# Performance work log

Hardware: AMD Instinct MI355X
Metric: run time of the kernel (lower is better)

Reference implementation:

```python
import jax, jax.numpy as jnp
import numpy as np

EMBED = 1024
B, S = 4, 4096

def setup_inputs() -> dict:
    key = jax.random.key(0)
    ks = jax.random.split(key, 7)
    std = 1.0 / np.sqrt(EMBED)
    X = jax.random.normal(ks[0], (B, S, EMBED), dtype=jnp.float32)
    Wq = jax.random.uniform(ks[1], (EMBED, EMBED), jnp.float32, -std, std)
    bq = jax.random.uniform(ks[2], (EMBED,), jnp.float32, -std, std)
    Wk = jax.random.uniform(ks[3], (EMBED, EMBED), jnp.float32, -std, std)
    bk = jax.random.uniform(ks[4], (EMBED,), jnp.float32, -std, std)
    Wv = jax.random.uniform(ks[5], (EMBED, EMBED), jnp.float32, -std, std)
    bv = jax.random.uniform(ks[6], (EMBED,), jnp.float32, -std, std)
    return {"X": X, "Wq": Wq, "bq": bq, "Wk": Wk, "bk": bk, "Wv": Wv, "bv": bv}

def reference(X, Wq, bq, Wk, bk, Wv, bv):
    # Linear layers (torch convention: x @ W.T + b)
    q = X @ Wq.T + bq  # [B, S, E]
    k = X @ Wk.T + bk
    v = X @ Wv.T + bv
    scale = 1.0 / jnp.sqrt(jnp.asarray(EMBED, X.dtype))
    scores = jnp.einsum('bse,bte->bst', q, k) * scale  # [B, S, S]
    weights = jax.nn.softmax(scores, axis=-1)
    return jnp.einsum('bst,bte->bse', weights, v)  # [B, S, E]
```

## Files before the change

kernel.cpp:

```cpp
#include <hip/hip_runtime.h>
#include <stdint.h>


typedef unsigned short ushort_t;
typedef __attribute__((ext_vector_type(8))) short short8;
typedef __attribute__((ext_vector_type(4))) float f32x4;

__device__ inline ushort_t f2bf(float f) {
  union { float f; unsigned u; } v; v.f = f;
  unsigned r = v.u + 0x7fffu + ((v.u >> 16) & 1u);
  return (ushort_t)(r >> 16);
}

__global__ __launch_bounds__(256) void zero_f32(float* __restrict__ p, int n) {
  int i = blockIdx.x * 256 + threadIdx.x;
  if (i < n) p[i] = 0.0f;
}

__global__ __launch_bounds__(256) void cvt_f32_bf16(
    const float* __restrict__ in, ushort_t* __restrict__ out, int n4) {
  int i = blockIdx.x * 256 + threadIdx.x;
  if (i < n4) {
    float4 v = ((const float4*)in)[i];
    ushort4 o;
    o.x = f2bf(v.x); o.y = f2bf(v.y); o.z = f2bf(v.z); o.w = f2bf(v.w);
    ((ushort4*)out)[i] = o;
  }
}

#define BM 256
#define BN 256
#define BK 64

template<int EPI>
__global__ __launch_bounds__(512, 2) void gemm_nt(
    const ushort_t* __restrict__ A, const ushort_t* __restrict__ B,
    const float* __restrict__ aux, const float* __restrict__ aux2,
    void* __restrict__ Cv,
    int K, int ldc, float scale, long sA, long sB, long sC,
    int lstride, float* __restrict__ lsum) {
  __shared__ ushort_t As[2][2][128 * 64];
  __shared__ ushort_t Bs[2][2][128 * 64];

  const int t = threadIdx.x;
  const int lane = t & 63;
  const int wave = t >> 6;
  const int wr = wave >> 2;
  const int wc = wave & 3;
  const int lr = lane & 15;
  const int quad = lane >> 4;

  const int gx = gridDim.x;
  const int nwg = gx * gridDim.y;
  const int lin = blockIdx.y * gx + blockIdx.x;
  const int swz = (lin & 7) * (nwg >> 3) + (lin >> 3);
  const int m0 = (swz / gx) * BM;
  const int n0 = (swz % gx) * BN;

  const long z = blockIdx.z;
  A += z * sA;
  B += z * sB;

  const int srow = t >> 3;
  const int scol = ((t & 7) ^ (srow & 7)) << 3;
  const ushort_t* pA = A + (size_t)(m0 + srow) * K + scol;
  const ushort_t* pB = B + (size_t)(n0 + srow) * K + scol;

  const int nkt = K / BK;

#define GLL(gp, lp) __builtin_amdgcn_global_load_lds( \
    (const __attribute__((address_space(1))) void*)(gp), \
    (__attribute__((address_space(3))) void*)(lp), 16, 0, 0)

#define STAGE_A(b, h, kt) do { if ((kt) < nkt) { \
    const ushort_t* g_ = pA + (size_t)(h) * 128 * K + (size_t)(kt) * BK; \
    GLL(g_, &As[b][h][t * 8]); \
    GLL(g_ + (size_t)64 * K, &As[b][h][(512 + t) * 8]); } } while (0)

#define STAGE_B(b, h, kt) do { if ((kt) < nkt) { \
    const ushort_t* g_ = pB + (size_t)(h) * 128 * K + (size_t)(kt) * BK; \
    GLL(g_, &Bs[b][h][t * 8]); \
    GLL(g_ + (size_t)64 * K, &Bs[b][h][(512 + t) * 8]); } } while (0)

  int aoff[4], boff[2];
#pragma unroll
  for (int mi = 0; mi < 4; ++mi)
    aoff[mi] = (wr * 64 + mi * 16 + lr) * 64 + ((quad ^ (lr & 7)) << 3);
#pragma unroll
  for (int ni = 0; ni < 2; ++ni)
    boff[ni] = (wc * 32 + ni * 16 + lr) * 64 + ((quad ^ (lr & 7)) << 3);

  f32x4 acc[8][4] = {};
  short8 af[4][2], bf[2][2];

#define LDA(b, mh) do { \
  _Pragma("unroll") for (int mi_ = 0; mi_ < 4; ++mi_) { \
    af[mi_][0] = *(const short8*)&As[b][mh][aoff[mi_]]; \
    af[mi_][1] = *(const short8*)&As[b][mh][aoff[mi_] ^ 32]; } } while (0)

#define LDB(b, nh) do { \
  _Pragma("unroll") for (int ni_ = 0; ni_ < 2; ++ni_) { \
    bf[ni_][0] = *(const short8*)&Bs[b][nh][boff[ni_]]; \
    bf[ni_][1] = *(const short8*)&Bs[b][nh][boff[ni_] ^ 32]; } } while (0)

#define MFMA16(mh, nh) do { \
  _Pragma("unroll") for (int mi_ = 0; mi_ < 4; ++mi_) \
  _Pragma("unroll") for (int ni_ = 0; ni_ < 2; ++ni_) { \
    acc[(mh) * 4 + mi_][(nh) * 2 + ni_] = __builtin_amdgcn_mfma_f32_16x16x32_bf16( \
        af[mi_][0], bf[ni_][0], acc[(mh) * 4 + mi_][(nh) * 2 + ni_], 0, 0, 0); \
    acc[(mh) * 4 + mi_][(nh) * 2 + ni_] = __builtin_amdgcn_mfma_f32_16x16x32_bf16( \
        af[mi_][1], bf[ni_][1], acc[(mh) * 4 + mi_][(nh) * 2 + ni_], 0, 0, 0); } } while (0)

#define PH_TAIL \
  __builtin_amdgcn_s_barrier(); \
  asm volatile("s_waitcnt lgkmcnt(0)" ::: "memory"); \
  __builtin_amdgcn_sched_barrier(0); \
  __builtin_amdgcn_s_setprio(1)

#define PH_END \
  __builtin_amdgcn_s_setprio(0); \
  __builtin_amdgcn_s_barrier()

  STAGE_A(0, 0, 0); STAGE_B(0, 0, 0); STAGE_A(0, 1, 0); STAGE_B(0, 1, 0);
  asm volatile("s_waitcnt vmcnt(4)" ::: "memory");
  STAGE_A(1, 0, 1); STAGE_B(1, 0, 1); STAGE_A(1, 1, 1);
  asm volatile("s_waitcnt vmcnt(6)" ::: "memory");
  __builtin_amdgcn_s_barrier();

  const int iters = nkt >> 1;
  for (int it = 0; it < iters; ++it) {
    const int T = it * 2;
    const bool last = (it == iters - 1);

    LDA(0, 0); LDB(0, 0);
    STAGE_B(1, 1, T + 1);
    PH_TAIL; MFMA16(0, 0); PH_END;

    LDB(0, 1);
    STAGE_A(0, 0, T + 2);
    PH_TAIL; MFMA16(0, 1); PH_END;

    LDA(0, 1); LDB(0, 0);
    STAGE_B(0, 0, T + 2);
    PH_TAIL; MFMA16(1, 0); PH_END;

    LDB(0, 1);
    STAGE_A(0, 1, T + 2);
    PH_TAIL; MFMA16(1, 1);
    __builtin_amdgcn_s_setprio(0);
    if (last) asm volatile("s_waitcnt vmcnt(0)" ::: "memory");
    else      asm volatile("s_waitcnt vmcnt(6)" ::: "memory");
    __builtin_amdgcn_s_barrier();

    LDA(1, 0); LDB(1, 0);
    STAGE_B(0, 1, T + 2);
    PH_TAIL; MFMA16(0, 0); PH_END;

    LDB(1, 1);
    STAGE_A(1, 0, T + 3);
    PH_TAIL; MFMA16(0, 1); PH_END;

    LDA(1, 1); LDB(1, 0);
    STAGE_B(1, 0, T + 3);
    PH_TAIL; MFMA16(1, 0); PH_END;

    LDB(1, 1);
    STAGE_A(1, 1, T + 3);
    PH_TAIL; MFMA16(1, 1);
    __builtin_amdgcn_s_setprio(0);
    if (!last) asm volatile("s_waitcnt vmcnt(6)" ::: "memory");
    __builtin_amdgcn_s_barrier();
  }

  const float* bias = (EPI == 1 && z) ? aux2 : aux;
#pragma unroll
  for (int fm = 0; fm < 8; ++fm) {
#pragma unroll
    for (int r = 0; r < 4; ++r) {
      const int row = m0 + (fm >> 2) * 128 + wr * 64 + (fm & 3) * 16 + quad * 4 + r;
      float rs = 0.0f, rl = 0.0f;
      if (EPI == 4) rl = 1.0f / bias[(size_t)z * lstride + row];
#pragma unroll
      for (int fn = 0; fn < 4; ++fn) {
        const int col = n0 + (fn >> 1) * 128 + wc * 32 + (fn & 1) * 16 + lr;
        const size_t off = (size_t)(z * sC) + (size_t)row * ldc + col;
        float v = acc[fm][fn][r] * scale;
        if (EPI == 1) {
          ((ushort_t*)Cv)[off] = f2bf(v + bias[col]);
        } else if (EPI == 2) {
          ((ushort_t*)Cv)[off] = f2bf(v + bias[row]);
        } else if (EPI == 3) {
          float e = __expf(v);
          rs += e;
          ((ushort_t*)Cv)[off] = f2bf(e);
        } else {
          ((float*)Cv)[off] = v * rl;
        }
      }
      if (EPI == 3) {
        rs += __shfl_xor(rs, 1);
        rs += __shfl_xor(rs, 2);
        rs += __shfl_xor(rs, 4);
        rs += __shfl_xor(rs, 8);
        if (lr == 0)
          atomicAdd(&lsum[(size_t)z * lstride + row], rs);
      }
    }
  }
}

extern "C" void kernel_launch(void* const* d_in, const int* in_sizes, int n_in,
                              void* d_out, int out_size, void* d_ws,
                              size_t ws_size, hipStream_t stream) {
  const float* X  = (const float*)d_in[0];
  const float* Wq = (const float*)d_in[1];
  const float* bq = (const float*)d_in[2];
  const float* Wk = (const float*)d_in[3];
  const float* bk = (const float*)d_in[4];
  const float* Wv = (const float*)d_in[5];
  const float* bv = (const float*)d_in[6];
  float* out = (float*)d_out;

  const int Bn = 4, S = 4096, E = 1024;
  const long SE  = (long)S * E;
  const long BSE = (long)Bn * SE;
  const long SS  = (long)S * S;
  const long EE  = (long)E * E;

  const size_t need_batched =
      (size_t)(4 * SS + 3 * EE + 3 * BSE) * 2 + (size_t)Bn * S * 4;
  const bool batched = ws_size >= need_batched;

  const long front = batched ? 4 * SS : BSE;
  ushort_t* Xb  = (ushort_t*)d_ws;
  ushort_t* P   = (ushort_t*)d_ws;
  ushort_t* Wqb = (ushort_t*)d_ws + front;
  ushort_t* Wkb = Wqb + EE;
  ushort_t* Wvb = Wkb + EE;
  ushort_t* Qw  = Wvb + EE;
  ushort_t* Kw  = Qw + BSE;
  ushort_t* Vt  = Kw + BSE;
  float*    l   = (float*)(Vt + BSE);

  zero_f32<<<(Bn * S) / 256, 256, 0, stream>>>(l, Bn * S);

  cvt_f32_bf16<<<(int)(BSE / 1024), 256, 0, stream>>>(X, Xb, (int)(BSE / 4));
  cvt_f32_bf16<<<(int)(EE / 1024), 256, 0, stream>>>(Wq, Wqb, (int)(EE / 4));
  cvt_f32_bf16<<<(int)(EE / 1024), 256, 0, stream>>>(Wk, Wkb, (int)(EE / 4));
  cvt_f32_bf16<<<(int)(EE / 1024), 256, 0, stream>>>(Wv, Wvb, (int)(EE / 4));

  gemm_nt<1><<<dim3(E / BN, Bn * S / BM, 2), 512, 0, stream>>>(
      Xb, Wqb, bq, bk, Qw, E, E, 1.0f, 0, EE, BSE, 0, nullptr);

  gemm_nt<2><<<dim3(S / BN, E / BM, Bn), 512, 0, stream>>>(
      Wvb, Xb, bv, nullptr, Vt, E, S, 1.0f, 0, SE, SE, 0, nullptr);

  if (batched) {
    gemm_nt<3><<<dim3(S / BN, S / BM, Bn), 512, 0, stream>>>(
        Qw, Kw, nullptr, nullptr, P, E, S, 0.03125f, SE, SE, SS, S, l);
    gemm_nt<4><<<dim3(E / BN, S / BM, Bn), 512, 0, stream>>>(
        P, Vt, l, nullptr, out, S, E, 1.0f, SS, SE, SE, S, nullptr);
  } else {
    for (int b = 0; b < Bn; ++b) {
      gemm_nt<3><<<dim3(S / BN, S / BM), 512, 0, stream>>>(
          Qw + b * SE, Kw + b * SE, nullptr, nullptr, P, E, S, 0.03125f,
          0, 0, 0, 0, l + b * S);
      gemm_nt<4><<<dim3(E / BN, S / BM), 512, 0, stream>>>(
          P, Vt + b * SE, l + b * S, nullptr, out + b * SE, S, E, 1.0f,
          0, 0, 0, 0, nullptr);
    }
  }
}
```

Measured before the change: 537.3 us.

## Make GEMM kernel persistent with cross-tile prefetch and XCD-chunked scheduling

Converts the GEMM into a persistent kernel launched with 256 workgroups, each processing several output tiles in sequence. Global-to-LDS staging for the next tile begins during the tail of the current tile's K-loop, which hides the prologue load latency between tiles. Tiles are assigned in chunks per XCD for cache locality. It also switches to 32-bit byte offsets, reorders the staging so B halves are held in separate register buffers, and trims redundant LDS reads. The risks are higher register pressure, 32-bit offset overflow on large tensors, and load imbalance.

```diff
diff --git a/kernel.cpp b/kernel.cpp
--- a/kernel.cpp
+++ b/kernel.cpp
@@ -3,6 +3,7 @@
 
 
 typedef unsigned short ushort_t;
+typedef unsigned int uint_t;
 typedef __attribute__((ext_vector_type(8))) short short8;
 typedef __attribute__((ext_vector_type(4))) float f32x4;
 
@@ -38,7 +39,8 @@
     const float* __restrict__ aux, const float* __restrict__ aux2,
     void* __restrict__ Cv,
     int K, int ldc, float scale, long sA, long sB, long sC,
-    int lstride, float* __restrict__ lsum) {
+    int lstride, float* __restrict__ lsum,
+    int tn, int tm, int tz, int tpb) {
   __shared__ ushort_t As[2][2][128 * 64];
   __shared__ ushort_t Bs[2][2][128 * 64];
 
@@ -50,37 +52,64 @@
   const int lr = lane & 15;
   const int quad = lane >> 4;
 
-  const int gx = gridDim.x;
-  const int nwg = gx * gridDim.y;
-  const int lin = blockIdx.y * gx + blockIdx.x;
-  const int swz = (lin & 7) * (nwg >> 3) + (lin >> 3);
-  const int m0 = (swz / gx) * BM;
-  const int n0 = (swz % gx) * BN;
-
-  const long z = blockIdx.z;
-  A += z * sA;
-  B += z * sB;
+  const int Kb = K * 2;
+  const int nkt = K / BK;
+  const int niter = nkt >> 1;
 
   const int srow = t >> 3;
   const int scol = ((t & 7) ^ (srow & 7)) << 3;
-  const ushort_t* pA = A + (size_t)(m0 + srow) * K + scol;
-  const ushort_t* pB = B + (size_t)(n0 + srow) * K + scol;
-
-  const int nkt = K / BK;
+
+  const int NT = tn * tm * tz;
+  const int tmn = tn * tm;
+  const bool chunked = (gridDim.x == 256) && ((NT & 255) == 0);
+  const int xcd = blockIdx.x & 7, wblk = blockIdx.x >> 3;
+  const int cpx = NT >> 3;
+
+  auto calc = [&](int i, int& m0_, int& n0_, long& z_, uint_t& oa_, uint_t& ob_) {
+    const int lin = chunked ? (xcd * cpx + i * 32 + wblk)
+                            : ((int)blockIdx.x + i * (int)gridDim.x);
+    const int zz = lin / tmn;
+    const int r = lin - zz * tmn;
+    const int mi = r / tn;
+    const int ni = r - mi * tn;
+    m0_ = mi * BM; n0_ = ni * BN; z_ = zz;
+    oa_ = (uint_t)(((size_t)zz * (size_t)sA + (size_t)(m0_ + srow) * K + scol) * 2);
+    ob_ = (uint_t)(((size_t)zz * (size_t)sB + (size_t)(n0_ + srow) * K + scol) * 2);
+  };
+
+  int m0, n0, m0n, n0n;
+  long z, zn;
+  uint_t oA_cur, oB_cur, oA_nxt, oB_nxt;
+  calc(0, m0, n0, z, oA_cur, oB_cur);
+  bool have_next = (tpb > 1);
+  if (have_next) calc(1, m0n, n0n, zn, oA_nxt, oB_nxt);
+  else { m0n = m0; n0n = n0; zn = z; oA_nxt = oA_cur; oB_nxt = oB_cur; }
 
 #define GLL(gp, lp) __builtin_amdgcn_global_load_lds( \
     (const __attribute__((address_space(1))) void*)(gp), \
     (__attribute__((address_space(3))) void*)(lp), 16, 0, 0)
 
-#define STAGE_A(b, h, kt) do { if ((kt) < nkt) { \
-    const ushort_t* g_ = pA + (size_t)(h) * 128 * K + (size_t)(kt) * BK; \
-    GLL(g_, &As[b][h][t * 8]); \
-    GLL(g_ + (size_t)64 * K, &As[b][h][(512 + t) * 8]); } } while (0)
-
-#define STAGE_B(b, h, kt) do { if ((kt) < nkt) { \
-    const ushort_t* g_ = pB + (size_t)(h) * 128 * K + (size_t)(kt) * BK; \
-    GLL(g_, &Bs[b][h][t * 8]); \
-    GLL(g_ + (size_t)64 * K, &Bs[b][h][(512 + t) * 8]); } } while (0)
+#define STAGE_A(b, h, j) do { \
+    const int j_ = (j); \
+    const bool in_ = (j_ < nkt); \
+    if (in_ || have_next) { \
+      const uint_t o_ = (in_ ? (oA_cur + (uint_t)(j_ * 128)) \
+                             : (oA_nxt + (uint_t)((j_ - nkt) * 128))) \
+                        + (uint_t)((h) * 128 * Kb); \
+      const char* g_ = (const char*)A + o_; \
+      GLL(g_, &As[b][h][t * 8]); \
+      GLL(g_ + (size_t)64 * Kb, &As[b][h][(512 + t) * 8]); } } while (0)
+
+#define STAGE_B(b, h, j) do { \
+    const int j_ = (j); \
+    const bool in_ = (j_ < nkt); \
+    if (in_ || have_next) { \
+      const uint_t o_ = (in_ ? (oB_cur + (uint_t)(j_ * 128)) \
+                             : (oB_nxt + (uint_t)((j_ - nkt) * 128))) \
+                        + (uint_t)((h) * 128 * Kb); \
+      const char* g_ = (const char*)B + o_; \
+      GLL(g_, &Bs[b][h][t * 8]); \
+      GLL(g_ + (size_t)64 * Kb, &Bs[b][h][(512 + t) * 8]); } } while (0)
 
   int aoff[4], boff[2];
 #pragma unroll
@@ -91,7 +120,8 @@
     boff[ni] = (wc * 32 + ni * 16 + lr) * 64 + ((quad ^ (lr & 7)) << 3);
 
   f32x4 acc[8][4] = {};
-  short8 af[4][2], bf[2][2];
+  short8 af[4][2];
+  short8 bfr[2][2][2];
 
 #define LDA(b, mh) do { \
   _Pragma("unroll") for (int mi_ = 0; mi_ < 4; ++mi_) { \
@@ -100,16 +130,16 @@
 
 #define LDB(b, nh) do { \
   _Pragma("unroll") for (int ni_ = 0; ni_ < 2; ++ni_) { \
-    bf[ni_][0] = *(const short8*)&Bs[b][nh][boff[ni_]]; \
-    bf[ni_][1] = *(const short8*)&Bs[b][nh][boff[ni_] ^ 32]; } } while (0)
+    bfr[nh][ni_][0] = *(const short8*)&Bs[b][nh][boff[ni_]]; \
+    bfr[nh][ni_][1] = *(const short8*)&Bs[b][nh][boff[ni_] ^ 32]; } } while (0)
 
 #define MFMA16(mh, nh) do { \
   _Pragma("unroll") for (int mi_ = 0; mi_ < 4; ++mi_) \
   _Pragma("unroll") for (int ni_ = 0; ni_ < 2; ++ni_) { \
     acc[(mh) * 4 + mi_][(nh) * 2 + ni_] = __builtin_amdgcn_mfma_f32_16x16x32_bf16( \
-        af[mi_][0], bf[ni_][0], acc[(mh) * 4 + mi_][(nh) * 2 + ni_], 0, 0, 0); \
+        af[mi_][0], bfr[nh][ni_][0], acc[(mh) * 4 + mi_][(nh) * 2 + ni_], 0, 0, 0); \
     acc[(mh) * 4 + mi_][(nh) * 2 + ni_] = __builtin_amdgcn_mfma_f32_16x16x32_bf16( \
-        af[mi_][1], bf[ni_][1], acc[(mh) * 4 + mi_][(nh) * 2 + ni_], 0, 0, 0); } } while (0)
+        af[mi_][1], bfr[nh][ni_][1], acc[(mh) * 4 + mi_][(nh) * 2 + ni_], 0, 0, 0); } } while (0)
 
 #define PH_TAIL \
   __builtin_amdgcn_s_barrier(); \
@@ -121,90 +151,100 @@
   __builtin_amdgcn_s_setprio(0); \
   __builtin_amdgcn_s_barrier()
 
-  STAGE_A(0, 0, 0); STAGE_B(0, 0, 0); STAGE_A(0, 1, 0); STAGE_B(0, 1, 0);
-  asm volatile("s_waitcnt vmcnt(4)" ::: "memory");
-  STAGE_A(1, 0, 1); STAGE_B(1, 0, 1); STAGE_A(1, 1, 1);
+#define VM6_BAR \
+  __builtin_amdgcn_s_setprio(0); \
+  asm volatile("s_waitcnt vmcnt(6)" ::: "memory"); \
+  __builtin_amdgcn_s_barrier()
+
+  STAGE_A(0, 0, 0); STAGE_B(0, 0, 0); STAGE_B(0, 1, 0); STAGE_A(0, 1, 0);
+  STAGE_A(1, 0, 1); STAGE_B(1, 0, 1); STAGE_B(1, 1, 1);
   asm volatile("s_waitcnt vmcnt(6)" ::: "memory");
   __builtin_amdgcn_s_barrier();
 
-  const int iters = nkt >> 1;
-  for (int it = 0; it < iters; ++it) {
-    const int T = it * 2;
-    const bool last = (it == iters - 1);
-
-    LDA(0, 0); LDB(0, 0);
-    STAGE_B(1, 1, T + 1);
-    PH_TAIL; MFMA16(0, 0); PH_END;
-
-    LDB(0, 1);
-    STAGE_A(0, 0, T + 2);
-    PH_TAIL; MFMA16(0, 1); PH_END;
-
-    LDA(0, 1); LDB(0, 0);
-    STAGE_B(0, 0, T + 2);
-    PH_TAIL; MFMA16(1, 0); PH_END;
-
-    LDB(0, 1);
-    STAGE_A(0, 1, T + 2);
-    PH_TAIL; MFMA16(1, 1);
-    __builtin_amdgcn_s_setprio(0);
-    if (last) asm volatile("s_waitcnt vmcnt(0)" ::: "memory");
-    else      asm volatile("s_waitcnt vmcnt(6)" ::: "memory");
-    __builtin_amdgcn_s_barrier();
-
-    LDA(1, 0); LDB(1, 0);
-    STAGE_B(0, 1, T + 2);
-    PH_TAIL; MFMA16(0, 0); PH_END;
-
-    LDB(1, 1);
-    STAGE_A(1, 0, T + 3);
-    PH_TAIL; MFMA16(0, 1); PH_END;
-
-    LDA(1, 1); LDB(1, 0);
-    STAGE_B(1, 0, T + 3);
-    PH_TAIL; MFMA16(1, 0); PH_END;
-
-    LDB(1, 1);
-    STAGE_A(1, 1, T + 3);
-    PH_TAIL; MFMA16(1, 1);
-    __builtin_amdgcn_s_setprio(0);
-    if (!last) asm volatile("s_waitcnt vmcnt(6)" ::: "memory");
-    __builtin_amdgcn_s_barrier();
-  }
-
-  const float* bias = (EPI == 1 && z) ? aux2 : aux;
-#pragma unroll
-  for (int fm = 0; fm < 8; ++fm) {
-#pragma unroll
-    for (int r = 0; r < 4; ++r) {
-      const int row = m0 + (fm >> 2) * 128 + wr * 64 + (fm & 3) * 16 + quad * 4 + r;
-      float rs = 0.0f, rl = 0.0f;
-      if (EPI == 4) rl = 1.0f / bias[(size_t)z * lstride + row];
-#pragma unroll
-      for (int fn = 0; fn < 4; ++fn) {
-        const int col = n0 + (fn >> 1) * 128 + wc * 32 + (fn & 1) * 16 + lr;
-        const size_t off = (size_t)(z * sC) + (size_t)row * ldc + col;
-        float v = acc[fm][fn][r] * scale;
-        if (EPI == 1) {
-          ((ushort_t*)Cv)[off] = f2bf(v + bias[col]);
-        } else if (EPI == 2) {
-          ((ushort_t*)Cv)[off] = f2bf(v + bias[row]);
-        } else if (EPI == 3) {
-          float e = __expf(v);
-          rs += e;
-          ((ushort_t*)Cv)[off] = f2bf(e);
-        } else {
-          ((float*)Cv)[off] = v * rl;
+  for (int tile = 0; tile < tpb; ++tile) {
+    for (int itl = 0; itl < niter; ++itl) {
+      const int T = itl * 2;
+
+      LDA(0, 0); LDB(0, 0);
+      STAGE_A(1, 1, T + 1);
+      PH_TAIL; MFMA16(0, 0); PH_END;
+
+      LDB(0, 1);
+      STAGE_A(0, 0, T + 2);
+      PH_TAIL; MFMA16(0, 1); PH_END;
+
+      LDA(0, 1);
+      STAGE_B(0, 0, T + 2);
+      PH_TAIL; MFMA16(1, 0); PH_END;
+
+      STAGE_B(0, 1, T + 2);
+      PH_TAIL; MFMA16(1, 1);
+      VM6_BAR;
+
+      LDA(1, 0); LDB(1, 0);
+      STAGE_A(0, 1, T + 2);
+      PH_TAIL; MFMA16(0, 0); PH_END;
+
+      LDB(1, 1);
+      STAGE_A(1, 0, T + 3);
+      PH_TAIL; MFMA16(0, 1); PH_END;
+
+      LDA(1, 1);
+      STAGE_B(1, 0, T + 3);
+      PH_TAIL; MFMA16(1, 0); PH_END;
+
+      STAGE_B(1, 1, T + 3);
+      PH_TAIL; MFMA16(1, 1);
+      VM6_BAR;
+    }
+
+    {
+      const float* bias = (EPI == 1 && z) ? aux2 : aux;
+#pragma unroll
+      for (int fm = 0; fm < 8; ++fm) {
+#pragma unroll
+        for (int r = 0; r < 4; ++r) {
+          const int row = m0 + (fm >> 2) * 128 + wr * 64 + (fm & 3) * 16 + quad * 4 + r;
+          float rs = 0.0f, rl = 0.0f;
+          if (EPI == 4) rl = 1.0f / bias[(size_t)z * lstride + row];
+#pragma unroll
+          for (int fn = 0; fn < 4; ++fn) {
+            const int col = n0 + (fn >> 1) * 128 + wc * 32 + (fn & 1) * 16 + lr;
+            const size_t off = (size_t)(z * sC) + (size_t)row * ldc + col;
+            float v = acc[fm][fn][r] * scale;
+            if (EPI == 1) {
+              ((ushort_t*)Cv)[off] = f2bf(v + bias[col]);
+            } else if (EPI == 2) {
+              ((ushort_t*)Cv)[off] = f2bf(v + bias[row]);
+            } else if (EPI == 3) {
+              float e = __expf(v);
+              rs += e;
+              ((ushort_t*)Cv)[off] = f2bf(e);
+            } else {
+              ((float*)Cv)[off] = v * rl;
+            }
+          }
+          if (EPI == 3) {
+            rs += __shfl_xor(rs, 1);
+            rs += __shfl_xor(rs, 2);
+            rs += __shfl_xor(rs, 4);
+            rs += __shfl_xor(rs, 8);
+            if (lr == 0)
+              atomicAdd(&lsum[(size_t)z * lstride + row], rs);
+          }
         }
       }
-      if (EPI == 3) {
-        rs += __shfl_xor(rs, 1);
-        rs += __shfl_xor(rs, 2);
-        rs += __shfl_xor(rs, 4);
-        rs += __shfl_xor(rs, 8);
-        if (lr == 0)
-          atomicAdd(&lsum[(size_t)z * lstride + row], rs);
-      }
+    }
+
+    if (tile + 1 < tpb) {
+      m0 = m0n; n0 = n0n; z = zn; oA_cur = oA_nxt; oB_cur = oB_nxt;
+      if (tile + 2 < tpb) calc(tile + 2, m0n, n0n, zn, oA_nxt, oB_nxt);
+      have_next = (tile + 2 < tpb);
+#pragma unroll
+      for (int fm = 0; fm < 8; ++fm)
+#pragma unroll
+        for (int fn = 0; fn < 4; ++fn)
+          acc[fm][fn] = (f32x4){0.0f, 0.0f, 0.0f, 0.0f};
     }
   }
 }
@@ -249,25 +289,29 @@
   cvt_f32_bf16<<<(int)(EE / 1024), 256, 0, stream>>>(Wk, Wkb, (int)(EE / 4));
   cvt_f32_bf16<<<(int)(EE / 1024), 256, 0, stream>>>(Wv, Wvb, (int)(EE / 4));
 
-  gemm_nt<1><<<dim3(E / BN, Bn * S / BM, 2), 512, 0, stream>>>(
-      Xb, Wqb, bq, bk, Qw, E, E, 1.0f, 0, EE, BSE, 0, nullptr);
-
-  gemm_nt<2><<<dim3(S / BN, E / BM, Bn), 512, 0, stream>>>(
-      Wvb, Xb, bv, nullptr, Vt, E, S, 1.0f, 0, SE, SE, 0, nullptr);
+  gemm_nt<1><<<256, 512, 0, stream>>>(
+      Xb, Wqb, bq, bk, Qw, E, E, 1.0f, 0, EE, BSE, 0, nullptr,
+      E / BN, Bn * S / BM, 2, 2);
+
+  gemm_nt<2><<<256, 512, 0, stream>>>(
+      Wvb, Xb, bv, nullptr, Vt, E, S, 1.0f, 0, SE, SE, 0, nullptr,
+      S / BN, E / BM, Bn, 1);
 
   if (batched) {
-    gemm_nt<3><<<dim3(S / BN, S / BM, Bn), 512, 0, stream>>>(
-        Qw, Kw, nullptr, nullptr, P, E, S, 0.03125f, SE, SE, SS, S, l);
-    gemm_nt<4><<<dim3(E / BN, S / BM, Bn), 512, 0, stream>>>(
-        P, Vt, l, nullptr, out, S, E, 1.0f, SS, SE, SE, S, nullptr);
+    gemm_nt<3><<<256, 512, 0, stream>>>(
+        Qw, Kw, nullptr, nullptr, P, E, S, 0.03125f, SE, SE, SS, S, l,
+        S / BN, S / BM, Bn, 4);
+    gemm_nt<4><<<256, 512, 0, stream>>>(
+        P, Vt, l, nullptr, out, S, E, 1.0f, SS, SE, SE, S, nullptr,
+        E / BN, S / BM, Bn, 1);
   } else {
     for (int b = 0; b < Bn; ++b) {
-      gemm_nt<3><<<dim3(S / BN, S / BM), 512, 0, stream>>>(
+      gemm_nt<3><<<256, 512, 0, stream>>>(
           Qw + b * SE, Kw + b * SE, nullptr, nullptr, P, E, S, 0.03125f,
-          0, 0, 0, 0, l + b * S);
-      gemm_nt<4><<<dim3(E / BN, S / BM), 512, 0, stream>>>(
+          0, 0, 0, 0, l + b * S, S / BN, S / BM, 1, 1);
+      gemm_nt<4><<<64, 512, 0, stream>>>(
           P, Vt + b * SE, l + b * S, nullptr, out + b * SE, S, E, 1.0f,
-          0, 0, 0, 0, nullptr);
+          0, 0, 0, 0, nullptr, E / BN, S / BM, 1, 1);
     }
   }
 }
```

Result: no change. 536.4 us (-0.2%).
